# Performance work log

Hardware: AMD Instinct MI355X
Metric: run time of the kernel (lower is better)

The kernel has to match this reference:

```python
import jax, jax.numpy as jnp
import numpy as np

N = 50000
E = 800000
D_IN, D_HID, D_OUT = 128, 128, 256


def _sage_layer(x, src, dst, W_l, b_l, W_r):
    # PyG SAGEConv: out = lin_l(mean_j x_j) + lin_r(x_i)
    msg = x[src]                                              # [E, d]
    agg = jax.ops.segment_sum(msg, dst, num_segments=x.shape[0])
    cnt = jax.ops.segment_sum(jnp.ones((src.shape[0],), x.dtype), dst,
                              num_segments=x.shape[0])
    mean = agg / jnp.maximum(cnt, 1.0)[:, None]
    return mean @ W_l.T + b_l + x @ W_r.T


def setup_inputs() -> dict:
    key = jax.random.key(0)
    ks = jax.random.split(key, 12)
    x = jax.random.normal(ks[0], (N, D_IN), dtype=jnp.float32)
    edge_index = jax.random.randint(ks[1], (2, E), 0, N, dtype=jnp.int64)

    def lin(k, out_d, in_d):
        s = 1.0 / np.sqrt(in_d)
        return jax.random.uniform(k, (out_d, in_d), jnp.float32, -s, s)

    return {
        "x": x,
        "edge_index": edge_index,
        "W_l0": lin(ks[2], D_HID, D_IN),
        "b_l0": jnp.zeros((D_HID,), jnp.float32),
        "W_r0": lin(ks[3], D_HID, D_IN),
        "W_l1": lin(ks[4], D_HID, D_HID),
        "b_l1": jnp.zeros((D_HID,), jnp.float32),
        "W_r1": lin(ks[5], D_HID, D_HID),
        "W_l2": lin(ks[6], D_OUT, D_HID),
        "b_l2": jnp.zeros((D_OUT,), jnp.float32),
        "W_r2": lin(ks[7], D_OUT, D_HID),
    }


def reference(x, edge_index, W_l0, b_l0, W_r0, W_l1, b_l1, W_r1, W_l2, b_l2, W_r2):
    src, dst = edge_index[0], edge_index[1]
    h = jax.nn.relu(_sage_layer(x, src, dst, W_l0, b_l0, W_r0))   # dropout = identity (eval)
    h = jax.nn.relu(_sage_layer(h, src, dst, W_l1, b_l1, W_r1))
    out = _sage_layer(h, src, dst, W_l2, b_l2, W_r2)
    return out
```

## Files before the change

kernel.cpp:

```cpp
#include <hip/hip_runtime.h>
#include <stdint.h>

typedef unsigned short u16;
typedef unsigned int   u32;
typedef __attribute__((ext_vector_type(8))) short short8;
typedef __attribute__((ext_vector_type(4))) float f32x4;

#define CHUNK 8192

__device__ __forceinline__ u16 f2bf(float f) {
    u32 u = __float_as_uint(f);
    u32 r = (u + 0x7FFFu + ((u >> 16) & 1u)) >> 16;
    return (u16)r;
}

__device__ __forceinline__ int edge_is64(const int* __restrict__ ei) {
    return ((ei[1] | ei[3] | ei[5] | ei[7] | ei[9] | ei[11]) == 0) ? 1 : 0;
}

__global__ void zero_out(float* __restrict__ p, size_t n) {
    size_t i = (size_t)blockIdx.x * 256 + threadIdx.x;
    size_t stride = (size_t)gridDim.x * 256;
    for (; i < n; i += stride) p[i] = 0.f;
}

__global__ void hist_bucket(const int* __restrict__ ei, int* __restrict__ cnt,
                            int E, int N, int nb, int NBK) {
    __shared__ int h[256];
    int b = blockIdx.x, t = threadIdx.x;
    h[t] = 0;
    __syncthreads();
    int is64 = edge_is64(ei);
    int base = b * CHUNK;
    int endE = min(base + CHUNK, E);
    for (int i = base + t; i < endE; i += 256) {
        int dst = is64 ? ei[2 * E + 2 * i] : ei[E + i];
        dst = min(max(dst, 0), N - 1);
        atomicAdd(&h[dst >> 8], 1);
    }
    __syncthreads();
    for (int B = t; B < NBK; B += 256) cnt[B * nb + b] = h[B];
}

__global__ void scan_partial(const int* __restrict__ a, int* __restrict__ bsum, int M) {
    __shared__ int sh[256];
    int t = threadIdx.x;
    int idx0 = blockIdx.x * 1024 + t * 4;
    int s = 0;
    #pragma unroll
    for (int i = 0; i < 4; ++i) { int idx = idx0 + i; if (idx < M) s += a[idx]; }
    sh[t] = s;
    __syncthreads();
    #pragma unroll
    for (int off = 128; off > 0; off >>= 1) {
        if (t < off) sh[t] += sh[t + off];
        __syncthreads();
    }
    if (t == 0) bsum[blockIdx.x] = sh[0];
}

__global__ void scan_bsum(int* __restrict__ bsum, int nbs) {
    __shared__ int sh[256];
    __shared__ int carry;
    int t = threadIdx.x;
    if (t == 0) carry = 0;
    __syncthreads();
    for (int base = 0; base < nbs; base += 256) {
        int v = (base + t < nbs) ? bsum[base + t] : 0;
        sh[t] = v;
        __syncthreads();
        #pragma unroll
        for (int off = 1; off < 256; off <<= 1) {
            int x = (t >= off) ? sh[t - off] : 0;
            __syncthreads();
            sh[t] += x;
            __syncthreads();
        }
        if (base + t < nbs) bsum[base + t] = carry + sh[t] - v;
        __syncthreads();
        if (t == 255) carry += sh[255];
        __syncthreads();
    }
}

__global__ void scan_final(int* __restrict__ a, const int* __restrict__ bsum, int M) {
    __shared__ int sh[256];
    int t = threadIdx.x;
    int idx0 = blockIdx.x * 1024 + t * 4;
    int v[4];
    int s = 0;
    #pragma unroll
    for (int i = 0; i < 4; ++i) {
        int idx = idx0 + i;
        v[i] = (idx < M) ? a[idx] : 0;
        s += v[i];
    }
    sh[t] = s;
    __syncthreads();
    #pragma unroll
    for (int off = 1; off < 256; off <<= 1) {
        int x = (t >= off) ? sh[t - off] : 0;
        __syncthreads();
        sh[t] += x;
        __syncthreads();
    }
    int run = sh[t] - s + bsum[blockIdx.x];
    #pragma unroll
    for (int i = 0; i < 4; ++i) {
        int idx = idx0 + i;
        if (idx < M) a[idx] = run;
        run += v[i];
    }
}

__global__ void scatter_pairs(const int* __restrict__ ei, const int* __restrict__ pboff,
                              u32* __restrict__ pairs, int E, int N, int nb, int NBK) {
    __shared__ int cur[256];
    int b = blockIdx.x, t = threadIdx.x;
    for (int B = t; B < NBK; B += 256) cur[B] = pboff[B * nb + b];
    __syncthreads();
    int is64 = edge_is64(ei);
    int base = b * CHUNK;
    int endE = min(base + CHUNK, E);
    for (int i = base + t; i < endE; i += 256) {
        int src = is64 ? ei[2 * i] : ei[i];
        int dst = is64 ? ei[2 * E + 2 * i] : ei[E + i];
        src = min(max(src, 0), N - 1);
        dst = min(max(dst, 0), N - 1);
        int slot = atomicAdd(&cur[dst >> 8], 1);
        pairs[slot] = (u32)src | ((u32)(dst & 255) << 17);
    }
}

__global__ void fine_sort(const u32* __restrict__ pairs, const int* __restrict__ pboff,
                          int* __restrict__ offs, int* __restrict__ ssrc,
                          int E, int N, int nb, int NBK) {
    __shared__ int hist[256];
    __shared__ int excl[256];
    __shared__ int cur[256];
    int B = blockIdx.x, t = threadIdx.x;
    if (B == 0 && t == 0) offs[N] = E;
    int rs = pboff[B * nb];
    int re = (B + 1 < NBK) ? pboff[(B + 1) * nb] : E;
    hist[t] = 0;
    __syncthreads();
    for (int i = rs + t; i < re; i += 256) {
        u32 p = pairs[i];
        atomicAdd(&hist[(p >> 17) & 255], 1);
    }
    __syncthreads();
    int v = hist[t];
    excl[t] = v;
    __syncthreads();
    #pragma unroll
    for (int off = 1; off < 256; off <<= 1) {
        int x = (t >= off) ? excl[t - off] : 0;
        __syncthreads();
        excl[t] += x;
        __syncthreads();
    }
    int ex = excl[t] - v;
    int node = B * 256 + t;
    if (node < N) offs[node] = rs + ex;
    cur[t] = rs + ex;
    __syncthreads();
    for (int i = rs + t; i < re; i += 256) {
        u32 p = pairs[i];
        int slot = atomicAdd(&cur[(p >> 17) & 255], 1);
        ssrc[slot] = (int)(p & 0x1FFFFu);
    }
}

__global__ void conv_bf16(const float4* __restrict__ x, uint2* __restrict__ H, int n4) {
    int i = blockIdx.x * 256 + threadIdx.x;
    if (i >= n4) return;
    float4 v = x[i];
    uint2 o;
    o.x = ((u32)f2bf(v.y) << 16) | f2bf(v.x);
    o.y = ((u32)f2bf(v.w) << 16) | f2bf(v.z);
    H[i] = o;
}

__global__ void prep_w_all(const float* __restrict__ Wl0, const float* __restrict__ Wr0,
                           const float* __restrict__ Wl1, const float* __restrict__ Wr1,
                           const float* __restrict__ Wl2, const float* __restrict__ Wr2,
                           u16* __restrict__ Wc0, u16* __restrict__ Wc1,
                           u16* __restrict__ Wc2) {
    int i = blockIdx.x * 256 + threadIdx.x;
    const float* Wl; const float* Wr; u16* Wc; int base;
    if (i < 32768)      { Wl = Wl0; Wr = Wr0; Wc = Wc0; base = i; }
    else if (i < 65536) { Wl = Wl1; Wr = Wr1; Wc = Wc1; base = i - 32768; }
    else                { Wl = Wl2; Wr = Wr2; Wc = Wc2; base = i - 65536; }
    int j = base >> 8, k = base & 255;
    float v = (k < 128) ? Wl[j * 128 + k] : Wr[j * 128 + (k - 128)];
    Wc[base] = f2bf(v);
}

__device__ __forceinline__ void acc8(float* a, uint4 p) {
    a[0] += __uint_as_float(p.x << 16); a[1] += __uint_as_float(p.x & 0xFFFF0000u);
    a[2] += __uint_as_float(p.y << 16); a[3] += __uint_as_float(p.y & 0xFFFF0000u);
    a[4] += __uint_as_float(p.z << 16); a[5] += __uint_as_float(p.z & 0xFFFF0000u);
    a[6] += __uint_as_float(p.w << 16); a[7] += __uint_as_float(p.w & 0xFFFF0000u);
}

__global__ void aggregate(const u16* __restrict__ H, const int* __restrict__ offs,
                          const int* __restrict__ ssrc, u16* __restrict__ M, int N) {
    int node = blockIdx.x * 16 + (threadIdx.x >> 4);
    int sub  = threadIdx.x & 15;
    if (node >= N) return;
    int beg = offs[node], end = offs[node + 1];
    float a0[8] = {}, a1[8] = {}, a2[8] = {}, a3[8] = {};
    int j = beg;
    for (; j + 3 < end; j += 4) {
        int s0 = ssrc[j], s1 = ssrc[j + 1], s2 = ssrc[j + 2], s3 = ssrc[j + 3];
        uint4 p0 = *(const uint4*)(H + (size_t)s0 * 128 + sub * 8);
        uint4 p1 = *(const uint4*)(H + (size_t)s1 * 128 + sub * 8);
        uint4 p2 = *(const uint4*)(H + (size_t)s2 * 128 + sub * 8);
        uint4 p3 = *(const uint4*)(H + (size_t)s3 * 128 + sub * 8);
        acc8(a0, p0); acc8(a1, p1); acc8(a2, p2); acc8(a3, p3);
    }
    for (; j < end; ++j) {
        uint4 p0 = *(const uint4*)(H + (size_t)ssrc[j] * 128 + sub * 8);
        acc8(a0, p0);
    }
    int d = end - beg;
    float sc = 1.f / (float)(d > 0 ? d : 1);
    #pragma unroll
    for (int i = 0; i < 8; ++i) a0[i] = (a0[i] + a1[i] + a2[i] + a3[i]) * sc;
    uint4 o;
    o.x = ((u32)f2bf(a0[1]) << 16) | f2bf(a0[0]);
    o.y = ((u32)f2bf(a0[3]) << 16) | f2bf(a0[2]);
    o.z = ((u32)f2bf(a0[5]) << 16) | f2bf(a0[4]);
    o.w = ((u32)f2bf(a0[7]) << 16) | f2bf(a0[6]);
    *(uint4*)(M + (size_t)node * 128 + sub * 8) = o;
}

template<int DOUT, bool RELU, bool OUT_F32>
__global__ __launch_bounds__(256, 3)
void gemm_mfma(const u16* __restrict__ M, const u16* __restrict__ H,
               const u16* __restrict__ Wc, const float* __restrict__ bias,
               void* __restrict__ out, int N) {
    int tid  = threadIdx.x;
    int w    = tid >> 6;
    int l    = tid & 63;
    int m_base = blockIdx.x * 128 + w * 32;
    int n_base = blockIdx.y * 128;

    int lr = l & 15;
    int lq = l >> 4;
    int kof = lq * 8;

    int r0 = m_base + lr, r1 = r0 + 16;
    const short8 zf = (short8){0,0,0,0,0,0,0,0};

    short8 a[2][8];
    #pragma unroll
    for (int ks = 0; ks < 8; ++ks) {
        const u16* Asrc = (ks < 4) ? M : H;
        int ka = (ks & 3) * 32 + kof;
        a[0][ks] = (r0 < N) ? *(const short8*)(Asrc + (size_t)r0 * 128 + ka) : zf;
        a[1][ks] = (r1 < N) ? *(const short8*)(Asrc + (size_t)r1 * 128 + ka) : zf;
    }

    f32x4 acc[2][8];
    #pragma unroll
    for (int i = 0; i < 2; ++i)
        #pragma unroll
        for (int j = 0; j < 8; ++j) acc[i][j] = (f32x4){0.f, 0.f, 0.f, 0.f};

    #pragma unroll
    for (int ks = 0; ks < 8; ++ks) {
        int kb = ks * 32 + kof;
        #pragma unroll
        for (int ct = 0; ct < 8; ++ct) {
            int wrow = n_base + ct * 16 + lr;
            short8 b = *(const short8*)(Wc + (size_t)wrow * 256 + kb);
            acc[0][ct] = __builtin_amdgcn_mfma_f32_16x16x32_bf16(a[0][ks], b, acc[0][ct], 0, 0, 0);
            acc[1][ct] = __builtin_amdgcn_mfma_f32_16x16x32_bf16(a[1][ks], b, acc[1][ct], 0, 0, 0);
        }
    }

    #pragma unroll
    for (int rg = 0; rg < 2; ++rg) {
        #pragma unroll
        for (int ct = 0; ct < 8; ++ct) {
            int col = n_base + ct * 16 + lr;
            float bv = bias[col];
            #pragma unroll
            for (int i = 0; i < 4; ++i) {
                int row = m_base + rg * 16 + lq * 4 + i;
                if (row >= N) continue;
                float v = acc[rg][ct][i] + bv;
                if (RELU) v = fmaxf(v, 0.f);
                if (OUT_F32) ((float*)out)[(size_t)row * DOUT + col] = v;
                else         ((u16*)out)[(size_t)row * DOUT + col] = f2bf(v);
            }
        }
    }
}

extern "C" void kernel_launch(void* const* d_in, const int* in_sizes, int n_in,
                              void* d_out, int out_size, void* d_ws, size_t ws_size,
                              hipStream_t stream) {
    const float* x   = (const float*)d_in[0];
    const int*   ei  = (const int*)d_in[1];
    const float* Wl0 = (const float*)d_in[2];
    const float* bl0 = (const float*)d_in[3];
    const float* Wr0 = (const float*)d_in[4];
    const float* Wl1 = (const float*)d_in[5];
    const float* bl1 = (const float*)d_in[6];
    const float* Wr1 = (const float*)d_in[7];
    const float* Wl2 = (const float*)d_in[8];
    const float* bl2 = (const float*)d_in[9];
    const float* Wr2 = (const float*)d_in[10];

    const int N = in_sizes[0] / 128;
    const int E = in_sizes[1] / 2;

    const int NBK = (N + 255) >> 8;
    const int nb  = (E + CHUNK - 1) / CHUNK;
    const int M_  = NBK * nb;
    const int nbs = (M_ + 1023) / 1024;

    size_t off = 0;
    auto alloc = [&](size_t bytes) -> size_t {
        size_t p = off;
        off += (bytes + 255) & ~(size_t)255;
        return p;
    };
    size_t o_cnt   = alloc((size_t)M_ * 4);
    size_t o_bsum  = alloc((size_t)nbs * 4);
    size_t o_offs  = alloc(((size_t)N + 1) * 4);
    size_t o_ssrc  = alloc((size_t)E * 4);
    size_t o_pairs = alloc((size_t)E * 4);
    size_t o_Hx    = alloc((size_t)N * 128 * 2);
    size_t o_Ha    = alloc((size_t)N * 128 * 2);
    size_t o_Hb    = alloc((size_t)N * 128 * 2);
    size_t o_Mb    = alloc((size_t)N * 128 * 2);
    size_t o_Wc0   = alloc((size_t)128 * 256 * 2);
    size_t o_Wc1   = alloc((size_t)128 * 256 * 2);
    size_t o_Wc2   = alloc((size_t)256 * 256 * 2);

    if (off > ws_size || NBK > 256 || N > (1 << 17)) {
        zero_out<<<2048, 256, 0, stream>>>((float*)d_out, (size_t)out_size);
        return;
    }

    char* ws = (char*)d_ws;
    int*  cnt   = (int*)(ws + o_cnt);
    int*  bsum  = (int*)(ws + o_bsum);
    int*  offs  = (int*)(ws + o_offs);
    int*  ssrc  = (int*)(ws + o_ssrc);
    u32*  pairs = (u32*)(ws + o_pairs);
    u16*  Hx    = (u16*)(ws + o_Hx);
    u16*  Ha    = (u16*)(ws + o_Ha);
    u16*  Hb    = (u16*)(ws + o_Hb);
    u16*  Mb    = (u16*)(ws + o_Mb);
    u16*  Wc0   = (u16*)(ws + o_Wc0);
    u16*  Wc1   = (u16*)(ws + o_Wc1);
    u16*  Wc2   = (u16*)(ws + o_Wc2);

    hist_bucket<<<nb, 256, 0, stream>>>(ei, cnt, E, N, nb, NBK);
    scan_partial<<<nbs, 256, 0, stream>>>(cnt, bsum, M_);
    scan_bsum<<<1, 256, 0, stream>>>(bsum, nbs);
    scan_final<<<nbs, 256, 0, stream>>>(cnt, bsum, M_);
    scatter_pairs<<<nb, 256, 0, stream>>>(ei, cnt, pairs, E, N, nb, NBK);
    fine_sort<<<NBK, 256, 0, stream>>>(pairs, cnt, offs, ssrc, E, N, nb, NBK);

    int n4 = N * 32;
    conv_bf16<<<(n4 + 255) / 256, 256, 0, stream>>>((const float4*)x, (uint2*)Hx, n4);
    prep_w_all<<<512, 256, 0, stream>>>(Wl0, Wr0, Wl1, Wr1, Wl2, Wr2, Wc0, Wc1, Wc2);

    int ab = (N + 15) / 16;
    dim3 g1((N + 127) / 128, 1), g2((N + 127) / 128, 2);

    aggregate<<<ab, 256, 0, stream>>>(Hx, offs, ssrc, Mb, N);
    gemm_mfma<128, true, false><<<g1, 256, 0, stream>>>(Mb, Hx, Wc0, bl0, Ha, N);
    aggregate<<<ab, 256, 0, stream>>>(Ha, offs, ssrc, Mb, N);
    gemm_mfma<128, true, false><<<g1, 256, 0, stream>>>(Mb, Ha, Wc1, bl1, Hb, N);
    aggregate<<<ab, 256, 0, stream>>>(Hb, offs, ssrc, Mb, N);
    gemm_mfma<256, false, true><<<g2, 256, 0, stream>>>(Mb, Hb, Wc2, bl2, d_out, N);
}
```

Measured before the change: 354.3 us.

## Fuse neighbor aggregation into MFMA GEMM via LDS staging per layer

Merges the separate aggregate and gemm kernels into one per-layer kernel. Each wave gathers and averages neighbor rows for its 32 nodes into LDS, then loads them as MFMA A operands, so the bf16 mean matrix never makes a round trip through global memory. The last layer loops over both 128-column halves in one block instead of using a second grid column. The trade-off is fewer blocks (391 vs many small aggregate blocks), so there is less parallelism to hide the gather latency, and the gather no longer overlaps across separate launches.

```diff
diff --git a/kernel.cpp b/kernel.cpp
--- a/kernel.cpp
+++ b/kernel.cpp
@@ -203,97 +203,110 @@
     a[6] += __uint_as_float(p.w << 16); a[7] += __uint_as_float(p.w & 0xFFFF0000u);
 }
 
-__global__ void aggregate(const u16* __restrict__ H, const int* __restrict__ offs,
-                          const int* __restrict__ ssrc, u16* __restrict__ M, int N) {
-    int node = blockIdx.x * 16 + (threadIdx.x >> 4);
-    int sub  = threadIdx.x & 15;
-    if (node >= N) return;
-    int beg = offs[node], end = offs[node + 1];
-    float a0[8] = {}, a1[8] = {}, a2[8] = {}, a3[8] = {};
-    int j = beg;
-    for (; j + 3 < end; j += 4) {
-        int s0 = ssrc[j], s1 = ssrc[j + 1], s2 = ssrc[j + 2], s3 = ssrc[j + 3];
-        uint4 p0 = *(const uint4*)(H + (size_t)s0 * 128 + sub * 8);
-        uint4 p1 = *(const uint4*)(H + (size_t)s1 * 128 + sub * 8);
-        uint4 p2 = *(const uint4*)(H + (size_t)s2 * 128 + sub * 8);
-        uint4 p3 = *(const uint4*)(H + (size_t)s3 * 128 + sub * 8);
-        acc8(a0, p0); acc8(a1, p1); acc8(a2, p2); acc8(a3, p3);
-    }
-    for (; j < end; ++j) {
-        uint4 p0 = *(const uint4*)(H + (size_t)ssrc[j] * 128 + sub * 8);
-        acc8(a0, p0);
-    }
-    int d = end - beg;
-    float sc = 1.f / (float)(d > 0 ? d : 1);
-    #pragma unroll
-    for (int i = 0; i < 8; ++i) a0[i] = (a0[i] + a1[i] + a2[i] + a3[i]) * sc;
-    uint4 o;
-    o.x = ((u32)f2bf(a0[1]) << 16) | f2bf(a0[0]);
-    o.y = ((u32)f2bf(a0[3]) << 16) | f2bf(a0[2]);
-    o.z = ((u32)f2bf(a0[5]) << 16) | f2bf(a0[4]);
-    o.w = ((u32)f2bf(a0[7]) << 16) | f2bf(a0[6]);
-    *(uint4*)(M + (size_t)node * 128 + sub * 8) = o;
-}
-
-template<int DOUT, bool RELU, bool OUT_F32>
+template<int NH, bool RELU, bool OUT_F32>
 __global__ __launch_bounds__(256, 3)
-void gemm_mfma(const u16* __restrict__ M, const u16* __restrict__ H,
-               const u16* __restrict__ Wc, const float* __restrict__ bias,
-               void* __restrict__ out, int N) {
-    int tid  = threadIdx.x;
-    int w    = tid >> 6;
-    int l    = tid & 63;
+void sage_fused(const u16* __restrict__ H, const u16* __restrict__ Wc,
+                const float* __restrict__ bias, const int* __restrict__ offs,
+                const int* __restrict__ ssrc, void* __restrict__ out, int N) {
+    __shared__ u16 lds[4][32][136];
+    const int DOUT = NH * 128;
+    int tid = threadIdx.x, w = tid >> 6, l = tid & 63;
+    int lq = l >> 4, sub = l & 15;
     int m_base = blockIdx.x * 128 + w * 32;
-    int n_base = blockIdx.y * 128;
+
+    for (int pass = 0; pass < 8; ++pass) {
+        int rloc = pass * 4 + lq;
+        int node = m_base + rloc;
+        float a0[8] = {}, a1[8] = {};
+        if (node < N) {
+            int beg = offs[node], end = offs[node + 1];
+            int j = beg;
+            for (; j + 7 < end; j += 8) {
+                uint4 p0 = *(const uint4*)(H + (size_t)ssrc[j    ] * 128 + sub * 8);
+                uint4 p1 = *(const uint4*)(H + (size_t)ssrc[j + 1] * 128 + sub * 8);
+                uint4 p2 = *(const uint4*)(H + (size_t)ssrc[j + 2] * 128 + sub * 8);
+                uint4 p3 = *(const uint4*)(H + (size_t)ssrc[j + 3] * 128 + sub * 8);
+                uint4 p4 = *(const uint4*)(H + (size_t)ssrc[j + 4] * 128 + sub * 8);
+                uint4 p5 = *(const uint4*)(H + (size_t)ssrc[j + 5] * 128 + sub * 8);
+                uint4 p6 = *(const uint4*)(H + (size_t)ssrc[j + 6] * 128 + sub * 8);
+                uint4 p7 = *(const uint4*)(H + (size_t)ssrc[j + 7] * 128 + sub * 8);
+                acc8(a0, p0); acc8(a1, p1); acc8(a0, p2); acc8(a1, p3);
+                acc8(a0, p4); acc8(a1, p5); acc8(a0, p6); acc8(a1, p7);
+            }
+            for (; j + 1 < end; j += 2) {
+                uint4 p0 = *(const uint4*)(H + (size_t)ssrc[j    ] * 128 + sub * 8);
+                uint4 p1 = *(const uint4*)(H + (size_t)ssrc[j + 1] * 128 + sub * 8);
+                acc8(a0, p0); acc8(a1, p1);
+            }
+            if (j < end) {
+                uint4 p0 = *(const uint4*)(H + (size_t)ssrc[j] * 128 + sub * 8);
+                acc8(a0, p0);
+            }
+            int d = end - beg;
+            float sc = 1.f / (float)(d > 0 ? d : 1);
+            #pragma unroll
+            for (int i = 0; i < 8; ++i) a0[i] = (a0[i] + a1[i]) * sc;
+        }
+        uint4 o;
+        o.x = ((u32)f2bf(a0[1]) << 16) | f2bf(a0[0]);
+        o.y = ((u32)f2bf(a0[3]) << 16) | f2bf(a0[2]);
+        o.z = ((u32)f2bf(a0[5]) << 16) | f2bf(a0[4]);
+        o.w = ((u32)f2bf(a0[7]) << 16) | f2bf(a0[6]);
+        *(uint4*)&lds[w][rloc][sub * 8] = o;
+    }
 
     int lr = l & 15;
-    int lq = l >> 4;
-    int kof = lq * 8;
-
     int r0 = m_base + lr, r1 = r0 + 16;
-    const short8 zf = (short8){0,0,0,0,0,0,0,0};
-
+    const short8 zf = (short8){0, 0, 0, 0, 0, 0, 0, 0};
     short8 a[2][8];
     #pragma unroll
-    for (int ks = 0; ks < 8; ++ks) {
-        const u16* Asrc = (ks < 4) ? M : H;
-        int ka = (ks & 3) * 32 + kof;
-        a[0][ks] = (r0 < N) ? *(const short8*)(Asrc + (size_t)r0 * 128 + ka) : zf;
-        a[1][ks] = (r1 < N) ? *(const short8*)(Asrc + (size_t)r1 * 128 + ka) : zf;
-    }
-
-    f32x4 acc[2][8];
-    #pragma unroll
-    for (int i = 0; i < 2; ++i)
+    for (int ks = 0; ks < 4; ++ks) {
+        int ka = ks * 32 + lq * 8;
+        a[0][ks] = *(const short8*)&lds[w][lr     ][ka];
+        a[1][ks] = *(const short8*)&lds[w][lr + 16][ka];
+    }
+    #pragma unroll
+    for (int ks = 4; ks < 8; ++ks) {
+        int ka = (ks - 4) * 32 + lq * 8;
+        a[0][ks] = (r0 < N) ? *(const short8*)(H + (size_t)r0 * 128 + ka) : zf;
+        a[1][ks] = (r1 < N) ? *(const short8*)(H + (size_t)r1 * 128 + ka) : zf;
+    }
+
+    #pragma unroll
+    for (int h = 0; h < NH; ++h) {
+        f32x4 acc[2][8];
         #pragma unroll
-        for (int j = 0; j < 8; ++j) acc[i][j] = (f32x4){0.f, 0.f, 0.f, 0.f};
-
-    #pragma unroll
-    for (int ks = 0; ks < 8; ++ks) {
-        int kb = ks * 32 + kof;
+        for (int i = 0; i < 2; ++i)
+            #pragma unroll
+            for (int j = 0; j < 8; ++j) acc[i][j] = (f32x4){0.f, 0.f, 0.f, 0.f};
+
         #pragma unroll
-        for (int ct = 0; ct < 8; ++ct) {
-            int wrow = n_base + ct * 16 + lr;
-            short8 b = *(const short8*)(Wc + (size_t)wrow * 256 + kb);
-            acc[0][ct] = __builtin_amdgcn_mfma_f32_16x16x32_bf16(a[0][ks], b, acc[0][ct], 0, 0, 0);
-            acc[1][ct] = __builtin_amdgcn_mfma_f32_16x16x32_bf16(a[1][ks], b, acc[1][ct], 0, 0, 0);
+        for (int ks = 0; ks < 8; ++ks) {
+            int kb = ks * 32 + lq * 8;
+            #pragma unroll
+            for (int ct = 0; ct < 8; ++ct) {
+                int wrow = h * 128 + ct * 16 + lr;
+                short8 b = *(const short8*)(Wc + (size_t)wrow * 256 + kb);
+                acc[0][ct] = __builtin_amdgcn_mfma_f32_16x16x32_bf16(a[0][ks], b, acc[0][ct], 0, 0, 0);
+                acc[1][ct] = __builtin_amdgcn_mfma_f32_16x16x32_bf16(a[1][ks], b, acc[1][ct], 0, 0, 0);
+            }
         }
-    }
-
-    #pragma unroll
-    for (int rg = 0; rg < 2; ++rg) {
+
         #pragma unroll
-        for (int ct = 0; ct < 8; ++ct) {
-            int col = n_base + ct * 16 + lr;
-            float bv = bias[col];
+        for (int rg = 0; rg < 2; ++rg) {
             #pragma unroll
-            for (int i = 0; i < 4; ++i) {
-                int row = m_base + rg * 16 + lq * 4 + i;
-                if (row >= N) continue;
-                float v = acc[rg][ct][i] + bv;
-                if (RELU) v = fmaxf(v, 0.f);
-                if (OUT_F32) ((float*)out)[(size_t)row * DOUT + col] = v;
-                else         ((u16*)out)[(size_t)row * DOUT + col] = f2bf(v);
+            for (int ct = 0; ct < 8; ++ct) {
+                int col = h * 128 + ct * 16 + lr;
+                float bv = bias[col];
+                #pragma unroll
+                for (int i = 0; i < 4; ++i) {
+                    int row = m_base + rg * 16 + lq * 4 + i;
+                    if (row >= N) continue;
+                    float v = acc[rg][ct][i] + bv;
+                    if (RELU) v = fmaxf(v, 0.f);
+                    if (OUT_F32) ((float*)out)[(size_t)row * DOUT + col] = v;
+                    else         ((u16*)out)[(size_t)row * DOUT + col] = f2bf(v);
+                }
             }
         }
     }
@@ -336,7 +349,6 @@
     size_t o_Hx    = alloc((size_t)N * 128 * 2);
     size_t o_Ha    = alloc((size_t)N * 128 * 2);
     size_t o_Hb    = alloc((size_t)N * 128 * 2);
-    size_t o_Mb    = alloc((size_t)N * 128 * 2);
     size_t o_Wc0   = alloc((size_t)128 * 256 * 2);
     size_t o_Wc1   = alloc((size_t)128 * 256 * 2);
     size_t o_Wc2   = alloc((size_t)256 * 256 * 2);
@@ -355,7 +367,6 @@
     u16*  Hx    = (u16*)(ws + o_Hx);
     u16*  Ha    = (u16*)(ws + o_Ha);
     u16*  Hb    = (u16*)(ws + o_Hb);
-    u16*  Mb    = (u16*)(ws + o_Mb);
     u16*  Wc0   = (u16*)(ws + o_Wc0);
     u16*  Wc1   = (u16*)(ws + o_Wc1);
     u16*  Wc2   = (u16*)(ws + o_Wc2);
@@ -371,13 +382,8 @@
     conv_bf16<<<(n4 + 255) / 256, 256, 0, stream>>>((const float4*)x, (uint2*)Hx, n4);
     prep_w_all<<<512, 256, 0, stream>>>(Wl0, Wr0, Wl1, Wr1, Wl2, Wr2, Wc0, Wc1, Wc2);
 
-    int ab = (N + 15) / 16;
-    dim3 g1((N + 127) / 128, 1), g2((N + 127) / 128, 2);
-
-    aggregate<<<ab, 256, 0, stream>>>(Hx, offs, ssrc, Mb, N);
-    gemm_mfma<128, true, false><<<g1, 256, 0, stream>>>(Mb, Hx, Wc0, bl0, Ha, N);
-    aggregate<<<ab, 256, 0, stream>>>(Ha, offs, ssrc, Mb, N);
-    gemm_mfma<128, true, false><<<g1, 256, 0, stream>>>(Mb, Ha, Wc1, bl1, Hb, N);
-    aggregate<<<ab, 256, 0, stream>>>(Hb, offs, ssrc, Mb, N);
-    gemm_mfma<256, false, true><<<g2, 256, 0, stream>>>(Mb, Hb, Wc2, bl2, d_out, N);
-}
+    int g = (N + 127) / 128;
+    sage_fused<1, true,  false><<<g, 256, 0, stream>>>(Hx, Wc0, bl0, offs, ssrc, Ha, N);
+    sage_fused<1, true,  false><<<g, 256, 0, stream>>>(Ha, Wc1, bl1, offs, ssrc, Hb, N);
+    sage_fused<2, false, true ><<<g, 256, 0, stream>>>(Hb, Wc2, bl2, offs, ssrc, d_out, N);
+}
```

Result: no change. 359.7 us (+1.5%).
